# Kernel optimization log

Measured on AMD Instinct MI355X. Metric: run time of the kernel, lower is better.

## Reference

```python
import jax, jax.numpy as jnp
import numpy as np

CHEBY_K = 3

def _normalize_adj(A):
    # A: [B, N, N]
    A = jnp.maximum(A, 0.0)
    N = A.shape[-1]
    A = A + jnp.eye(N, dtype=A.dtype)[None, :, :]
    D = jnp.maximum(A.sum(-1), 1e-6)          # [B, N]
    D_inv_sqrt = D ** -0.5
    return D_inv_sqrt[..., :, None] * A * D_inv_sqrt[..., None, :]


def setup_inputs() -> dict:
    key = jax.random.key(0)
    k1, k2, k3, k4, k5 = jax.random.split(key, 5)
    B, N, F_in, F_out, E = 16, 512, 64, 64, 16
    x = jax.random.normal(k1, (B, N, F_in), dtype=jnp.float32)
    emb = jax.random.normal(k2, (B, N, E), dtype=jnp.float32)
    A = jax.random.uniform(k3, (B, N, N), dtype=jnp.float32)
    # xavier-uniform-like init for pools
    lim_w = float(np.sqrt(6.0 / (E * CHEBY_K * F_in + F_out)))
    weights_pool = jax.random.uniform(k4, (E, CHEBY_K, F_in, F_out), dtype=jnp.float32,
                                      minval=-lim_w, maxval=lim_w)
    lim_b = float(np.sqrt(6.0 / (E + F_out)))
    bias_pool = jax.random.uniform(k5, (E, F_out), dtype=jnp.float32,
                                   minval=-lim_b, maxval=lim_b)
    return {"x": x, "emb": emb, "A": A,
            "weights_pool": weights_pool, "bias_pool": bias_pool}


def reference(x, emb, A, weights_pool, bias_pool):
    B, N, F_in = x.shape
    K = CHEBY_K
    A_hat = _normalize_adj(A)                                   # [B,N,N]
    t0 = jnp.broadcast_to(jnp.eye(N, dtype=x.dtype)[None], (B, N, N))
    supports = [t0, A_hat]
    for _ in range(2, K):
        supports.append(2.0 * jnp.matmul(A_hat, supports[-1]) - supports[-2])
    supports = jnp.stack(supports, axis=1)                      # [B,K,N,N]
    x_g = jnp.einsum('bknm,bmf->bknf', supports, x)             # [B,K,N,F_in]
    # fused per-node adaptive conv: avoids materializing [B,K,N,F_in,F_out]
    out = jnp.einsum('bknf,bne,ekfo->bno', x_g, emb, weights_pool)
    out = out + jnp.einsum('bne,eo->bno', emb, bias_pool)       # [B,N,F_out]
    return out
```

## Files before the change

### kernel.cpp

```cpp
#include <hip/hip_runtime.h>
#include <hip/hip_bf16.h>

#define NB 16
#define NN 512
#define NF 64
#define NE 16
#define NKF 192
#define NNODE (NB*NN)

typedef __hip_bfloat16 bf16;
typedef __attribute__((ext_vector_type(8))) short short8;
typedef __attribute__((ext_vector_type(4))) float f32x4;

typedef const __attribute__((address_space(1))) char gchar;
typedef __attribute__((address_space(3))) char lchar;

__device__ inline void gload16(const void* g, void* l) {
    __builtin_amdgcn_global_load_lds((gchar*)g, (lchar*)l, 16, 0, 0);
}

__device__ inline short f2bs(float f) {
    union { bf16 b; short s; } u; u.b = __float2bfloat16(f); return u.s;
}

__global__ __launch_bounds__(256) void k_pre(
    const float* __restrict__ A, const float* __restrict__ x,
    const float* __restrict__ Wp, float* __restrict__ dis,
    bf16* __restrict__ xg, bf16* __restrict__ xT, bf16* __restrict__ Bt) {
    __shared__ float Ts[64][66];
    int bid = blockIdx.x, tid = threadIdx.x;
    if (bid < 2048) {
        int row = bid * 4 + (tid >> 6);
        int lane = tid & 63;
        const float4* a = (const float4*)(A + (size_t)row * NN);
        float s = 0.f;
        #pragma unroll
        for (int j = 0; j < 2; ++j) {
            float4 v = a[lane + 64 * j];
            s += fmaxf(v.x, 0.f) + fmaxf(v.y, 0.f) + fmaxf(v.z, 0.f) + fmaxf(v.w, 0.f);
        }
        #pragma unroll
        for (int off = 32; off >= 1; off >>= 1) s += __shfl_down(s, off, 64);
        if (lane == 0) dis[row] = rsqrtf(fmaxf(s + 1.0f, 1e-6f));
    } else if (bid < 2176) {
        int node0 = (bid - 2048) * 64;
        int r = tid >> 2, f0 = (tid & 3) * 16;
        const float* xp = x + (size_t)(node0 + r) * NF + f0;
        float v[16];
        #pragma unroll
        for (int i = 0; i < 16; ++i) v[i] = xp[i];
        short8 p0, p1;
        #pragma unroll
        for (int i = 0; i < 8; ++i) { p0[i] = f2bs(v[i]); p1[i] = f2bs(v[8 + i]); }
        *(short8*)&xg[(size_t)(node0 + r) * NKF + f0] = p0;
        *(short8*)&xg[(size_t)(node0 + r) * NKF + f0 + 8] = p1;
        #pragma unroll
        for (int i = 0; i < 4; ++i)
            *(float4*)&Ts[r][f0 + i * 4] = *(const float4*)(v + i * 4);
        __syncthreads();
        int f = tid >> 2, nq0 = (tid & 3) * 16;
        int b = node0 >> 9, nloc = node0 & (NN - 1);
        bf16* xt = xT + (size_t)(b * NF + f) * NN + nloc + nq0;
        #pragma unroll
        for (int h = 0; h < 2; ++h) {
            short8 o;
            #pragma unroll
            for (int i = 0; i < 8; ++i) o[i] = f2bs(Ts[nq0 + h * 8 + i][f]);
            *(short8*)&xt[h * 8] = o;
        }
    } else {
        int q = bid - 2176;
        int e = q / 3, kt = q % 3;
        int r = tid >> 2, o0 = (tid & 3) * 16;
        const float* wp = Wp + (size_t)e * (NKF * NF) + (size_t)(kt * 64 + r) * NF + o0;
        #pragma unroll
        for (int i = 0; i < 4; ++i)
            *(float4*)&Ts[r][o0 + i * 4] = *(const float4*)(wp + i * 4);
        __syncthreads();
        int o = tid >> 2, r0 = (tid & 3) * 16;
        bf16* bt = Bt + (size_t)(e * 64 + o) * NKF + kt * 64 + r0;
        #pragma unroll
        for (int h = 0; h < 2; ++h) {
            short8 w;
            #pragma unroll
            for (int i = 0; i < 8; ++i) w[i] = f2bs(Ts[r0 + h * 8 + i][o]);
            *(short8*)&bt[h * 8] = w;
        }
    }
}

__global__ __launch_bounds__(256) void k_ahat(
    const float* __restrict__ A, const float* __restrict__ dis,
    bf16* __restrict__ Ah) {
    int tid = threadIdx.x;
    int row = blockIdx.x * 4 + (tid >> 6);
    int m0 = (tid & 63) * 8;
    int b = row >> 9, n = row & (NN - 1);
    const float* db = dis + b * NN;
    float dn = db[n];
    const float* ap = A + (size_t)row * NN + m0;
    float4 a0 = *(const float4*)ap, a1 = *(const float4*)(ap + 4);
    float4 d0 = *(const float4*)(db + m0), d1 = *(const float4*)(db + m0 + 4);
    float av[8] = {a0.x, a0.y, a0.z, a0.w, a1.x, a1.y, a1.z, a1.w};
    float dm[8] = {d0.x, d0.y, d0.z, d0.w, d1.x, d1.y, d1.z, d1.w};
    short8 o;
    #pragma unroll
    for (int i = 0; i < 8; ++i) {
        float v = fmaxf(av[i], 0.f) + ((n == m0 + i) ? 1.f : 0.f);
        o[i] = f2bs(v * dn * dm[i]);
    }
    *(short8*)&Ah[(size_t)row * NN + m0] = o;
}

template <int PASS>
__global__ __launch_bounds__(256) void k_spmm(
    const short* __restrict__ Ah, const short* __restrict__ Bsrc,
    const float* __restrict__ x, bf16* __restrict__ xg, bf16* __restrict__ y1T) {
    __shared__ short As[4 * 1024];
    __shared__ short Xs[4 * 2048];
    __shared__ float Cs[32][66];
    int tid = threadIdx.x, lane = tid & 63, w = tid >> 6;
    int n0 = blockIdx.x * 32, b = blockIdx.y;
    const short* Ab = Ah + (size_t)b * NN * NN;
    const short* Xb = Bsrc + (size_t)b * NF * NN;

    int sr = tid >> 2;
    int p  = tid & 3;
    int cA = p ^ ((sr >> 1) & 3);
    int ar2 = (tid >> 2) & 31;
    int kq  = tid >> 7;
    int cA2 = p ^ ((ar2 >> 1) & 3);

    int fr = lane & 15, ak = lane >> 4;

    f32x4 acc[2] = {};

    for (int kt = 0; kt < 4; ++kt) {
        __syncthreads();
        #pragma unroll
        for (int h = 0; h < 2; ++h) {
            int kc = h * 2 + kq;
            gload16(Ab + (size_t)(n0 + ar2) * NN + kt * 128 + kc * 32 + cA2 * 8,
                    As + h * 2048 + tid * 8);
        }
        #pragma unroll
        for (int kc = 0; kc < 4; ++kc)
            gload16(Xb + (size_t)sr * NN + kt * 128 + kc * 32 + cA * 8,
                    Xs + kc * 2048 + tid * 8);
        __syncthreads();
        int ra = 16 * (w & 1) + fr;
        int swA = (ak ^ ((ra >> 1) & 3)) * 8;
        #pragma unroll
        for (int kc = 0; kc < 4; ++kc) {
            short8 afr = *(const short8*)&As[kc * 1024 + ra * 32 + swA];
            #pragma unroll
            for (int j2 = 0; j2 < 2; ++j2) {
                int cr = 32 * (w >> 1) + 16 * j2 + fr;
                short8 bfr = *(const short8*)&Xs[kc * 2048 + cr * 32 +
                                                 ((ak ^ ((cr >> 1) & 3)) * 8)];
                acc[j2] = __builtin_amdgcn_mfma_f32_16x16x32_bf16(afr, bfr, acc[j2], 0, 0, 0);
            }
        }
    }

    #pragma unroll
    for (int j2 = 0; j2 < 2; ++j2)
        #pragma unroll
        for (int r = 0; r < 4; ++r)
            Cs[16 * (w & 1) + 4 * ak + r][32 * (w >> 1) + 16 * j2 + fr] = acc[j2][r];
    __syncthreads();

    int nl = tid >> 3, f0 = (tid & 7) * 8;
    size_t node = (size_t)b * NN + n0 + nl;
    float cv[8];
    #pragma unroll
    for (int i = 0; i < 8; ++i) cv[i] = Cs[nl][f0 + i];
    if (PASS == 0) {
        short8 pk;
        #pragma unroll
        for (int i = 0; i < 8; ++i) pk[i] = f2bs(cv[i]);
        *(short8*)&xg[node * NKF + 64 + f0] = pk;
        int f = tid >> 2, nq0 = (tid & 3) * 8;
        short8 o;
        #pragma unroll
        for (int i = 0; i < 8; ++i) o[i] = f2bs(Cs[nq0 + i][f]);
        *(short8*)&y1T[(size_t)(b * NF + f) * NN + n0 + nq0] = o;
    } else {
        const float* xp = x + node * NF + f0;
        short8 pk;
        #pragma unroll
        for (int i = 0; i < 8; ++i) pk[i] = f2bs(2.f * cv[i] - xp[i]);
        *(short8*)&xg[node * NKF + 128 + f0] = pk;
    }
}

__global__ __launch_bounds__(256) void k_gemm(
    const short* __restrict__ xg, const short* __restrict__ Bt,
    bf16* __restrict__ t) {
    __shared__ short As[128 * 32];
    __shared__ short Bs[128 * 32];
    int tid = threadIdx.x;
    int lane = tid & 63;
    int w = tid >> 6;
    int n0 = blockIdx.x * 128;
    int c0 = blockIdx.y * 128;

    int rA0 = tid >> 2;
    int p   = tid & 3;
    int cA  = p ^ ((rA0 >> 1) & 3);

    int fr = lane & 15;
    int fc = ((lane >> 4) ^ ((fr >> 1) & 3)) * 8;

    f32x4 acc[4][4] = {};

    for (int kt = 0; kt < 6; ++kt) {
        __syncthreads();
        gload16(xg + (size_t)(n0 + rA0) * NKF + kt * 32 + cA * 8, As + tid * 8);
        gload16(xg + (size_t)(n0 + rA0 + 64) * NKF + kt * 32 + cA * 8, As + 2048 + tid * 8);
        gload16(Bt + (size_t)(c0 + rA0) * NKF + kt * 32 + cA * 8, Bs + tid * 8);
        gload16(Bt + (size_t)(c0 + rA0 + 64) * NKF + kt * 32 + cA * 8, Bs + 2048 + tid * 8);
        __syncthreads();

        int wr = w >> 1, wc = w & 1;
        short8 a[4], bfr[4];
        #pragma unroll
        for (int i = 0; i < 4; ++i)
            a[i] = *(const short8*)&As[(wr * 64 + i * 16 + fr) * 32 + fc];
        #pragma unroll
        for (int j = 0; j < 4; ++j)
            bfr[j] = *(const short8*)&Bs[(wc * 64 + j * 16 + fr) * 32 + fc];
        #pragma unroll
        for (int i = 0; i < 4; ++i)
            #pragma unroll
            for (int j = 0; j < 4; ++j)
                acc[i][j] = __builtin_amdgcn_mfma_f32_16x16x32_bf16(a[i], bfr[j], acc[i][j], 0, 0, 0);
    }

    int wr = w >> 1, wc = w & 1;
    #pragma unroll
    for (int i = 0; i < 4; ++i) {
        #pragma unroll
        for (int j = 0; j < 4; ++j) {
            #pragma unroll
            for (int r = 0; r < 4; ++r) {
                int m = n0 + wr * 64 + i * 16 + (lane >> 4) * 4 + r;
                int cc = c0 + wc * 64 + j * 16 + (lane & 15);
                t[(size_t)m * 1024 + cc] = __float2bfloat16(acc[i][j][r]);
            }
        }
    }
}

__global__ void k_reduce(const bf16* __restrict__ t, const float* __restrict__ emb,
                         const float* __restrict__ bp, float* __restrict__ out) {
    int gid = blockIdx.x * 256 + threadIdx.x;
    int node = gid >> 6, o = gid & 63;
    float s = 0.f;
    #pragma unroll
    for (int e = 0; e < NE; ++e) {
        float tv = __bfloat162float(t[(size_t)node * 1024 + e * 64 + o]);
        s = fmaf(emb[(size_t)node * NE + e], tv + bp[e * 64 + o], s);
    }
    out[gid] = s;
}

extern "C" void kernel_launch(void* const* d_in, const int* in_sizes, int n_in,
                              void* d_out, int out_size, void* d_ws, size_t ws_size,
                              hipStream_t stream) {
    const float* x   = (const float*)d_in[0];
    const float* emb = (const float*)d_in[1];
    const float* A   = (const float*)d_in[2];
    const float* Wp  = (const float*)d_in[3];
    const float* bp  = (const float*)d_in[4];
    float* out = (float*)d_out;

    float* ws  = (float*)d_ws;
    float* dis = ws;
    bf16*  xT  = (bf16*)(ws + 8192);
    bf16*  y1T = (bf16*)(ws + 270336);
    bf16*  xg  = (bf16*)(ws + 532480);
    bf16*  Bt  = (bf16*)(ws + 1318912);
    bf16*  Ah  = (bf16*)(ws + 1417216);
    bf16*  t   = (bf16*)(ws + 3514368);

    k_pre<<<2224, 256, 0, stream>>>(A, x, Wp, dis, xg, xT, Bt);
    k_ahat<<<2048, 256, 0, stream>>>(A, dis, Ah);
    dim3 g2(NN / 32, NB);
    k_spmm<0><<<g2, 256, 0, stream>>>((const short*)Ah, (const short*)xT, x, xg, y1T);
    k_spmm<1><<<g2, 256, 0, stream>>>((const short*)Ah, (const short*)y1T, x, xg, y1T);
    dim3 gg(NNODE / 128, 8);
    k_gemm<<<gg, 256, 0, stream>>>((const short*)xg, (const short*)Bt, t);
    k_reduce<<<NNODE * NF / 256, 256, 0, stream>>>(t, emb, bp, out);
}
```

Before: 39.46 us.

## Fuse adjacency normalization into SpMM tile loads, drop k_ahat kernel

```diff
diff --git a/kernel.cpp b/kernel.cpp
--- a/kernel.cpp
+++ b/kernel.cpp
@@ -89,47 +89,30 @@
     }
 }
 
-__global__ __launch_bounds__(256) void k_ahat(
-    const float* __restrict__ A, const float* __restrict__ dis,
-    bf16* __restrict__ Ah) {
-    int tid = threadIdx.x;
-    int row = blockIdx.x * 4 + (tid >> 6);
-    int m0 = (tid & 63) * 8;
-    int b = row >> 9, n = row & (NN - 1);
-    const float* db = dis + b * NN;
-    float dn = db[n];
-    const float* ap = A + (size_t)row * NN + m0;
-    float4 a0 = *(const float4*)ap, a1 = *(const float4*)(ap + 4);
-    float4 d0 = *(const float4*)(db + m0), d1 = *(const float4*)(db + m0 + 4);
-    float av[8] = {a0.x, a0.y, a0.z, a0.w, a1.x, a1.y, a1.z, a1.w};
-    float dm[8] = {d0.x, d0.y, d0.z, d0.w, d1.x, d1.y, d1.z, d1.w};
-    short8 o;
-    #pragma unroll
-    for (int i = 0; i < 8; ++i) {
-        float v = fmaxf(av[i], 0.f) + ((n == m0 + i) ? 1.f : 0.f);
-        o[i] = f2bs(v * dn * dm[i]);
-    }
-    *(short8*)&Ah[(size_t)row * NN + m0] = o;
-}
-
 template <int PASS>
 __global__ __launch_bounds__(256) void k_spmm(
-    const short* __restrict__ Ah, const short* __restrict__ Bsrc,
-    const float* __restrict__ x, bf16* __restrict__ xg, bf16* __restrict__ y1T) {
+    const float* __restrict__ A, const float* __restrict__ dis,
+    const short* __restrict__ Bsrc, const float* __restrict__ x,
+    bf16* __restrict__ xg, bf16* __restrict__ y1T) {
     __shared__ short As[4 * 1024];
     __shared__ short Xs[4 * 2048];
     __shared__ float Cs[32][66];
     int tid = threadIdx.x, lane = tid & 63, w = tid >> 6;
     int n0 = blockIdx.x * 32, b = blockIdx.y;
-    const short* Ab = Ah + (size_t)b * NN * NN;
+    const float* Ab = A + (size_t)b * NN * NN;
+    const float* db = dis + b * NN;
     const short* Xb = Bsrc + (size_t)b * NF * NN;
 
     int sr = tid >> 2;
     int p  = tid & 3;
     int cA = p ^ ((sr >> 1) & 3);
-    int ar2 = (tid >> 2) & 31;
-    int kq  = tid >> 7;
-    int cA2 = p ^ ((ar2 >> 1) & 3);
+    int r_ = tid >> 3;
+    int q_ = tid & 7;
+    int c16 = q_ * 16;
+    float dn = db[n0 + r_];
+    int key = (r_ >> 1) & 3;
+    int kc_ = c16 >> 5;
+    int cb  = (c16 & 31) >> 3;
 
     int fr = lane & 15, ak = lane >> 4;
 
@@ -137,16 +120,39 @@
 
     for (int kt = 0; kt < 4; ++kt) {
         __syncthreads();
-        #pragma unroll
-        for (int h = 0; h < 2; ++h) {
-            int kc = h * 2 + kq;
-            gload16(Ab + (size_t)(n0 + ar2) * NN + kt * 128 + kc * 32 + cA2 * 8,
-                    As + h * 2048 + tid * 8);
-        }
         #pragma unroll
         for (int kc = 0; kc < 4; ++kc)
             gload16(Xb + (size_t)sr * NN + kt * 128 + kc * 32 + cA * 8,
                     Xs + kc * 2048 + tid * 8);
+        {
+            const float* ap = Ab + (size_t)(n0 + r_) * NN + kt * 128 + c16;
+            const float* dp = db + kt * 128 + c16;
+            float4 a4[4], d4[4];
+            #pragma unroll
+            for (int i = 0; i < 4; ++i) {
+                a4[i] = *(const float4*)(ap + 4 * i);
+                d4[i] = *(const float4*)(dp + 4 * i);
+            }
+            float av[16] = {a4[0].x, a4[0].y, a4[0].z, a4[0].w,
+                            a4[1].x, a4[1].y, a4[1].z, a4[1].w,
+                            a4[2].x, a4[2].y, a4[2].z, a4[2].w,
+                            a4[3].x, a4[3].y, a4[3].z, a4[3].w};
+            float dm[16] = {d4[0].x, d4[0].y, d4[0].z, d4[0].w,
+                            d4[1].x, d4[1].y, d4[1].z, d4[1].w,
+                            d4[2].x, d4[2].y, d4[2].z, d4[2].w,
+                            d4[3].x, d4[3].y, d4[3].z, d4[3].w};
+            int grow = n0 + r_, gcol0 = kt * 128 + c16;
+            short8 pk0, pk1;
+            #pragma unroll
+            for (int i = 0; i < 8; ++i) {
+                float v0 = fmaxf(av[i], 0.f) + ((grow == gcol0 + i) ? 1.f : 0.f);
+                pk0[i] = f2bs(v0 * dn * dm[i]);
+                float v1 = fmaxf(av[8 + i], 0.f) + ((grow == gcol0 + 8 + i) ? 1.f : 0.f);
+                pk1[i] = f2bs(v1 * dn * dm[8 + i]);
+            }
+            *(short8*)&As[kc_ * 1024 + r_ * 32 + ((cb    ) ^ key) * 8] = pk0;
+            *(short8*)&As[kc_ * 1024 + r_ * 32 + ((cb + 1) ^ key) * 8] = pk1;
+        }
         __syncthreads();
         int ra = 16 * (w & 1) + fr;
         int swA = (ak ^ ((ra >> 1) & 3)) * 8;
@@ -281,14 +287,12 @@
     bf16*  y1T = (bf16*)(ws + 270336);
     bf16*  xg  = (bf16*)(ws + 532480);
     bf16*  Bt  = (bf16*)(ws + 1318912);
-    bf16*  Ah  = (bf16*)(ws + 1417216);
-    bf16*  t   = (bf16*)(ws + 3514368);
+    bf16*  t   = (bf16*)(ws + 1417216);
 
     k_pre<<<2224, 256, 0, stream>>>(A, x, Wp, dis, xg, xT, Bt);
-    k_ahat<<<2048, 256, 0, stream>>>(A, dis, Ah);
     dim3 g2(NN / 32, NB);
-    k_spmm<0><<<g2, 256, 0, stream>>>((const short*)Ah, (const short*)xT, x, xg, y1T);
-    k_spmm<1><<<g2, 256, 0, stream>>>((const short*)Ah, (const short*)y1T, x, xg, y1T);
+    k_spmm<0><<<g2, 256, 0, stream>>>(A, dis, (const short*)xT, x, xg, y1T);
+    k_spmm<1><<<g2, 256, 0, stream>>>(A, dis, (const short*)y1T, x, xg, y1T);
     dim3 gg(NNODE / 128, 8);
     k_gemm<<<gg, 256, 0, stream>>>((const short*)xg, (const short*)Bt, t);
     k_reduce<<<NNODE * NF / 256, 256, 0, stream>>>(t, emb, bp, out);
```

Result: slower. 42.30 us (+7.2%).
